# Kernel tuning notes

Measured on AMD Instinct MI355X. Metric: run time of the kernel, lower is better.

Reference implementation:

```python
import jax, jax.numpy as jnp
import numpy as np

IOU_HI = 0.5
IOU_LO = 0.0
ROI_BS = 256
POS_RATIO = 0.25
BG = 20  # background class id; valid classes 0..BG-1
NUM_POS = int(ROI_BS * POS_RATIO)
DELTAS_SCALING = np.array([10.0, 10.0, 5.0, 5.0], dtype=np.float32)  # (x, y, w, h)


def _make_boxes(key, shape):
    ka, kb = jax.random.split(key)
    c = jax.random.uniform(ka, shape + (2,), minval=0.05, maxval=0.95)
    s = jax.random.uniform(kb, shape + (2,), minval=0.02, maxval=0.4)
    lo = jnp.clip(c - s / 2, 0.0, 1.0)
    hi = jnp.clip(c + s / 2, 0.0, 1.0)
    return jnp.concatenate([lo, hi], -1)  # (y1, x1, y2, x2), normalized


def setup_inputs() -> dict:
    key = jax.random.key(0)
    k1, k2, k3 = jax.random.split(key, 3)
    B, N, G = 32, 12000, 200
    rois = _make_boxes(k1, (B, N))
    gt_boxes = _make_boxes(k2, (B, G))
    # class == BG marks a padded / invalid GT box
    gt_class_ids = jax.random.randint(k3, (B, G), 0, BG + 1).astype(jnp.int32)
    return {"rois": rois, "gt_class_ids": gt_class_ids, "gt_boxes": gt_boxes}


def _iou(rois, gts):
    # rois [N,4], gts [G,4] in (y1,x1,y2,x2) -> [N,G]
    y1 = jnp.maximum(rois[:, None, 0], gts[None, :, 0])
    x1 = jnp.maximum(rois[:, None, 1], gts[None, :, 1])
    y2 = jnp.minimum(rois[:, None, 2], gts[None, :, 2])
    x2 = jnp.minimum(rois[:, None, 3], gts[None, :, 3])
    inter = jnp.clip(y2 - y1, 0.0) * jnp.clip(x2 - x1, 0.0)
    ar = (rois[:, 2] - rois[:, 0]) * (rois[:, 3] - rois[:, 1])
    ag = (gts[:, 2] - gts[:, 0]) * (gts[:, 3] - gts[:, 1])
    return inter / (ar[:, None] + ag[None, :] - inter + 1e-8)


def _encode(r, g):
    # (tx, ty, tw, th) * scaling, r/g: [K,4] in (y1,x1,y2,x2)
    eps = 1e-6
    rh = r[:, 2] - r[:, 0]; rw = r[:, 3] - r[:, 1]
    rcy = r[:, 0] + rh / 2; rcx = r[:, 1] + rw / 2
    gh = g[:, 2] - g[:, 0]; gw = g[:, 3] - g[:, 1]
    gcy = g[:, 0] + gh / 2; gcx = g[:, 1] + gw / 2
    tx = (gcx - rcx) / (rw + eps)
    ty = (gcy - rcy) / (rh + eps)
    tw = jnp.log(jnp.maximum(gw, eps) / (rw + eps))
    th = jnp.log(jnp.maximum(gh, eps) / (rh + eps))
    return jnp.stack([tx, ty, tw, th], -1) * jnp.asarray(DELTAS_SCALING)


def _per_image(rois, gt_cls, gt_boxes):
    iou = _iou(rois, gt_boxes)                       # [N,G]
    valid_gt = gt_cls < BG
    iou = jnp.where(valid_gt[None, :], iou, -1.0)
    max_iou = iou.max(1)                             # [N]
    best_gt = iou.argmax(1)                          # [N]
    pos = max_iou >= IOU_HI
    neg = (max_iou < IOU_HI) & (max_iou >= IOU_LO)

    # deterministic sampling: highest-IoU positives / negatives first
    pos_val, pos_idx = jax.lax.top_k(jnp.where(pos, max_iou, -1.0), NUM_POS)
    pos_ok = pos_val > 0.0
    neg_val, neg_idx = jax.lax.top_k(jnp.where(neg, max_iou + 2.0, -1.0), ROI_BS)
    neg_ok = neg_val > 0.0

    rP = jnp.arange(NUM_POS, dtype=jnp.float32)
    rN = jnp.arange(ROI_BS, dtype=jnp.float32)
    prio = jnp.concatenate([jnp.where(pos_ok, 1e9 - rP, -1e9 - rP),
                            jnp.where(neg_ok, 1e6 - rN, -1e6 - rN)])
    cand_idx = jnp.concatenate([pos_idx, neg_idx])
    cand_pos = jnp.concatenate([pos_ok, jnp.zeros(ROI_BS, bool)])
    _, sel = jax.lax.top_k(prio, ROI_BS)
    sel_roi = cand_idx[sel]                          # [ROI_BS]
    sel_is_pos = cand_pos[sel]                       # [ROI_BS]

    labels = jnp.where(sel_is_pos, gt_cls[best_gt[sel_roi]], BG)
    rois_sel = rois[sel_roi]                         # [ROI_BS,4]
    gts_sel = gt_boxes[best_gt[sel_roi]]             # [ROI_BS,4]
    t = _encode(rois_sel, gts_sel) * sel_is_pos[:, None].astype(rois.dtype)

    cls_onehot = jax.nn.one_hot(labels, BG + 1, dtype=rois.dtype)   # [ROI_BS,BG+1]
    onehot_fg = jax.nn.one_hot(labels, BG, dtype=rois.dtype)        # zero row for bg
    mask4 = jnp.repeat(onehot_fg, 4, axis=1)                        # [ROI_BS,4*BG]
    deltas_full = (onehot_fg[:, :, None] * t[:, None, :]).reshape(ROI_BS, 4 * BG)
    reg = jnp.concatenate([mask4, deltas_full], -1)                 # [ROI_BS,8*BG]
    return rois_sel, cls_onehot, reg


def reference(rois, gt_class_ids, gt_boxes):
    return jax.vmap(_per_image)(rois, gt_class_ids, gt_boxes)
```

## Files before the change

### kernel.cpp

```cpp
#include <hip/hip_runtime.h>
#include <stdint.h>

#pragma clang fp contract(off)

#define BATCH 32
#define NROI  12000
#define NGT   200
#define BGCLS 20
#define ROIBS 256
#define NPOS  64
#define NBIN  1024
#define CAP   1024
#define NPAD  256
#define TSEL  1024
#define HSH   16
#define HST   (NBIN + 2)

__device__ __forceinline__ void roi_maxiou_all(const float4* cbox, const float* carea,
                                               int nv, float ry1, float rx1,
                                               float ry2, float rx2,
                                               float& best, int& bj) {
#pragma clang fp contract(off)
  float ar = (ry2 - ry1) * (rx2 - rx1);
  best = -1.0f; bj = 0;
  for (int j = 0; j < nv; ++j) {
    float4 q = cbox[j];
    float yy1 = fmaxf(ry1, q.x);
    float xx1 = fmaxf(rx1, q.y);
    float yy2 = fminf(ry2, q.z);
    float xx2 = fminf(rx2, q.w);
    float inter = fmaxf(yy2 - yy1, 0.0f) * fmaxf(xx2 - xx1, 0.0f);
    float den = ((ar + carea[j]) - inter) + 1e-8f;
    float iou = inter / den;
    if (iou > best) { best = iou; bj = j; }
  }
}

__global__ __launch_bounds__(256) void k_ioumax(const float* __restrict__ rois,
                                                const int* __restrict__ gtc,
                                                const float* __restrict__ gtb,
                                                float* __restrict__ max_iou,
                                                int* __restrict__ best_j) {
#pragma clang fp contract(off)
  __shared__ float4 cbox[NPAD];
  __shared__ float carea[NPAD];
  __shared__ int snv, wtmp[4];
  const int b = blockIdx.y;
  const int tid = threadIdx.x;

  cbox[tid] = make_float4(2.f, 2.f, 2.f, 2.f);
  carea[tid] = 0.f;
  {
    bool valid = false; float4 p = make_float4(0.f, 0.f, 0.f, 0.f);
    if (tid < NGT) {
      p = *(const float4*)(gtb + ((size_t)b * NGT + tid) * 4);
      valid = gtc[(size_t)b * NGT + tid] < BGCLS;
    }
    unsigned long long m = __ballot(valid);
    int w = tid >> 6;
    if ((tid & 63) == 0) wtmp[w] = __popcll(m);
    __syncthreads();
    if (tid == 0) snv = wtmp[0] + wtmp[1] + wtmp[2] + wtmp[3];
    if (valid) {
      int off = 0;
      for (int i = 0; i < w; ++i) off += wtmp[i];
      int pos = off + __popcll(m & ((1ull << (tid & 63)) - 1ull));
      cbox[pos] = p;
      carea[pos] = (p.z - p.x) * (p.w - p.y);
    }
    __syncthreads();
  }
  const int nv = snv;

  int n = blockIdx.x * 256 + tid;
  if (n >= NROI) return;
  const float4 r = *(const float4*)(rois + ((size_t)b * NROI + n) * 4);
  const float ar = (r.z - r.x) * (r.w - r.y);
  float best = -1.0f; int bj = 0;
#pragma unroll 1
  for (int c = 0; c < 4; ++c) {
    unsigned long long m = 0ull;
#pragma unroll 8
    for (int j2 = 0; j2 < 64; ++j2) {
      float4 q = cbox[c * 64 + j2];
      bool ov = (fminf(r.z, q.z) > fmaxf(r.x, q.x)) &&
                (fminf(r.w, q.w) > fmaxf(r.y, q.y));
      m |= ((unsigned long long)ov) << j2;
    }
    while (m) {
      int j2 = __ffsll(m) - 1;
      m &= (m - 1);
      int j = c * 64 + j2;
      float4 q = cbox[j];
      float yy1 = fmaxf(r.x, q.x);
      float xx1 = fmaxf(r.y, q.y);
      float yy2 = fminf(r.z, q.z);
      float xx2 = fminf(r.w, q.w);
      float inter = fmaxf(yy2 - yy1, 0.0f) * fmaxf(xx2 - xx1, 0.0f);
      float den = ((ar + carea[j]) - inter) + 1e-8f;
      float iou = inter / den;
      if (iou > best) { best = iou; bj = j; }
    }
  }
  if (best < 0.0f && nv > 0) best = 0.0f;
  max_iou[(size_t)b * NROI + n] = best;
  best_j[(size_t)b * NROI + n] = bj;
}

template <bool USE_WS>
__global__ __launch_bounds__(TSEL) void k_sel(const float* __restrict__ rois,
                                              const int* __restrict__ gtc,
                                              const float* __restrict__ gtb,
                                              const float* __restrict__ max_iou,
                                              const int* __restrict__ best_j,
                                              float* __restrict__ out) {
#pragma clang fp contract(off)
  __shared__ float4 cbox[NGT];
  __shared__ float carea[NGT];
  __shared__ int ccls[NGT];
  __shared__ int snv, wtmp[16];
  __shared__ float val[NROI];
  __shared__ unsigned long long list[CAP];
  __shared__ int hs[HSH][HST];
  __shared__ int ss[NBIN];
  __shared__ int sel_r[ROIBS];
  __shared__ int scnt, sT;
  const int b = blockIdx.x;
  const int tid = threadIdx.x;

  {
    bool valid = false; float4 p = make_float4(0.f, 0.f, 0.f, 0.f); int cls = BGCLS;
    if (tid < NGT) {
      p = *(const float4*)(gtb + ((size_t)b * NGT + tid) * 4);
      cls = gtc[(size_t)b * NGT + tid];
      valid = (cls < BGCLS);
    }
    unsigned long long m = __ballot(valid);
    int w = tid >> 6;
    if ((tid & 63) == 0) wtmp[w] = __popcll(m);
    if (tid < ROIBS) sel_r[tid] = 0;
    __syncthreads();
    if (tid == 0) { int s = 0; for (int i = 0; i < 16; ++i) s += wtmp[i]; snv = s; }
    if (valid) {
      int off = 0;
      for (int i = 0; i < w; ++i) off += wtmp[i];
      int pos = off + __popcll(m & ((1ull << (tid & 63)) - 1ull));
      cbox[pos] = p;
      carea[pos] = (p.z - p.x) * (p.w - p.y);
      ccls[pos] = cls;
    }
    __syncthreads();
  }
  const int nv = snv;

  if constexpr (USE_WS) {
    for (int n = tid; n < NROI; n += TSEL) val[n] = max_iou[(size_t)b * NROI + n];
  } else {
    for (int n = tid; n < NROI; n += TSEL) {
      const float4 r = *(const float4*)(rois + ((size_t)b * NROI + n) * 4);
      float best; int bj;
      roi_maxiou_all(cbox, carea, nv, r.x, r.y, r.z, r.w, best, bj);
      val[n] = best;
    }
  }
  __syncthreads();

  auto phase = [&](bool isPos, int need, unsigned base, int shift,
                   float lo, float hi, int slotBase) -> int {
    for (int i = tid; i < HSH * HST; i += TSEL) ((int*)hs)[i] = 0;
    if (tid == 0) { scnt = 0; sT = 0; }
    __syncthreads();
    const int sh = tid & (HSH - 1);
    for (int n = tid; n < NROI; n += TSEL) {
      float v = val[n];
      if (v >= lo && v < hi) {
        float kv = isPos ? v : (v + 2.0f);
        int bin = min((int)((__float_as_uint(kv) - base) >> shift), NBIN - 1);
        atomicAdd(&hs[sh][bin], 1);
      }
    }
    __syncthreads();
    {
      int s = 0;
#pragma unroll
      for (int i = 0; i < HSH; ++i) s += hs[i][tid];
      ss[tid] = s;
    }
    __syncthreads();
    for (int off = 1; off < NBIN; off <<= 1) {
      int a = (tid + off < NBIN) ? ss[tid + off] : 0;
      __syncthreads();
      ss[tid] += a;
      __syncthreads();
    }
    {
      int nxt = (tid + 1 < NBIN) ? ss[tid + 1] : 0;
      if (ss[tid] >= need && nxt < need) sT = tid;
    }
    __syncthreads();
    const int T = sT;
    for (int n = tid; n < NROI; n += TSEL) {
      float v = val[n];
      if (v >= lo && v < hi) {
        unsigned kh = __float_as_uint(isPos ? v : (v + 2.0f));
        int bin = min((int)((kh - base) >> shift), NBIN - 1);
        if (bin >= T) {
          int idx = atomicAdd(&scnt, 1);
          if (idx < CAP)
            list[idx] = ((unsigned long long)kh << 32) | (unsigned)(0x7fffffff - n);
        }
      }
    }
    __syncthreads();
    const int cnt = min(scnt, CAP);
    const int limit = min(cnt, need);
    if (tid < cnt) {
      unsigned long long ki = list[tid];
      int rank = 0;
      for (int j = 0; j < cnt; ++j) rank += (list[j] > ki);
      if (rank < limit)
        sel_r[slotBase + rank] = 0x7fffffff - (int)(ki & 0xffffffffu);
    }
    __syncthreads();
    return limit;
  };

  const int P = phase(true, NPOS, 0x3F000000u, 13, 0.5f, 3.0f, 0);
  phase(false, ROIBS - P, 0x40000000u, 11, 0.0f, 0.5f, P);

  {
    const int slot = tid >> 2, q = tid & 3;
    const int r = sel_r[slot];
    const int isp = (slot < P) ? 1 : 0;
    const float4 rv = *(const float4*)(rois + ((size_t)b * NROI + r) * 4);
    float ry1 = rv.x, rx1 = rv.y, ry2 = rv.z, rx2 = rv.w;
    int bj;
    if constexpr (USE_WS) {
      bj = best_j[(size_t)b * NROI + r];
    } else {
      float bb;
      roi_maxiou_all(cbox, carea, nv, ry1, rx1, ry2, rx2, bb, bj);
    }
    int label = isp ? ccls[bj] : BGCLS;

    float* out1 = out;
    float* out2 = out + (size_t)BATCH * ROIBS * 4;
    float* out3 = out + (size_t)BATCH * ROIBS * 25;
    size_t row = (size_t)b * ROIBS + slot;

    if (q == 0) {
      *(float4*)(out1 + row * 4) = rv;
      float* o2 = out2 + row * 21;
      for (int c = 0; c <= BGCLS; ++c) o2[c] = (c == label) ? 1.0f : 0.0f;
    }

    float t0 = 0.f, t1 = 0.f, t2 = 0.f, t3 = 0.f;
    if (isp) {
      const float eps = 1e-6f;
      float4 g = cbox[bj];
      float gy1 = g.x, gx1 = g.y, gy2 = g.z, gx2 = g.w;
      float rh = ry2 - ry1, rw = rx2 - rx1;
      float rcy = ry1 + rh * 0.5f, rcx = rx1 + rw * 0.5f;
      float gh = gy2 - gy1, gw = gx2 - gx1;
      float gcy = gy1 + gh * 0.5f, gcx = gx1 + gw * 0.5f;
      t0 = ((gcx - rcx) / (rw + eps)) * 10.0f;
      t1 = ((gcy - rcy) / (rh + eps)) * 10.0f;
      t2 = logf(fmaxf(gw, eps) / (rw + eps)) * 5.0f;
      t3 = logf(fmaxf(gh, eps) / (rh + eps)) * 5.0f;
    }
    int m0 = label * 4;
    float* o3 = out3 + row * 160;
    for (int c = q * 10; c < q * 10 + 10; ++c) {
      float4 wv = make_float4(0.f, 0.f, 0.f, 0.f);
      if (isp) {
        float* wp = &wv.x;
#pragma unroll
        for (int jj = 0; jj < 4; ++jj) {
          int e = c * 4 + jj;
          float x = 0.f;
          if (e >= m0 && e < m0 + 4) x = 1.0f;
          int d = e - 80 - m0;
          if (d == 0) x = t0; else if (d == 1) x = t1;
          else if (d == 2) x = t2; else if (d == 3) x = t3;
          wp[jj] = x;
        }
      }
      *(float4*)(o3 + c * 4) = wv;
    }
  }
}

extern "C" void kernel_launch(void* const* d_in, const int* in_sizes, int n_in,
                              void* d_out, int out_size, void* d_ws, size_t ws_size,
                              hipStream_t stream) {
  const float* rois = (const float*)d_in[0];
  const int*   gtc  = (const int*)d_in[1];
  const float* gtb  = (const float*)d_in[2];
  float*       out  = (float*)d_out;

  size_t need = (size_t)BATCH * NROI * 8;
  if (d_ws && ws_size >= need) {
    float* mi = (float*)d_ws;
    int*   bj = (int*)d_ws + (size_t)BATCH * NROI;
    k_ioumax<<<dim3((NROI + 255) / 256, BATCH), 256, 0, stream>>>(rois, gtc, gtb, mi, bj);
    k_sel<true><<<BATCH, TSEL, 0, stream>>>(rois, gtc, gtb, mi, bj, out);
  } else {
    k_sel<false><<<BATCH, TSEL, 0, stream>>>(rois, gtc, gtb, nullptr, nullptr, out);
  }
}
```

Baseline: 100.7 us.

## Use fast-reciprocal dense IoU argmax with exact fallback and wave-level suffix scan

The IoU max kernel swaps the ballot-mask sparse overlap loop for a dense loop over the valid GT boxes. Each IoU is computed with a hardware reciprocal, and the kernel tracks the top two values. When the top two are too close to separate given the reciprocal's error, it recomputes exactly via roi_maxiou_all; otherwise it recomputes only the winner with a true division. The selection kernel replaces the 10-step shared-memory Hillis-Steele suffix scan, which needs two barriers per step, with a wavefront shuffle scan plus a 16-entry cross-wave combine. This cuts barriers and LDS traffic. The dense loop does more arithmetic than the sparse one and adds a divergent fallback path.

```diff
diff --git a/kernel.cpp b/kernel.cpp
--- a/kernel.cpp
+++ b/kernel.cpp
@@ -11,7 +11,6 @@
 #define NPOS  64
 #define NBIN  1024
 #define CAP   1024
-#define NPAD  256
 #define TSEL  1024
 #define HSH   16
 #define HST   (NBIN + 2)
@@ -42,14 +41,12 @@
                                                 float* __restrict__ max_iou,
                                                 int* __restrict__ best_j) {
 #pragma clang fp contract(off)
-  __shared__ float4 cbox[NPAD];
-  __shared__ float carea[NPAD];
+  __shared__ float4 cbox[NGT];
+  __shared__ float carea[NGT];
   __shared__ int snv, wtmp[4];
   const int b = blockIdx.y;
   const int tid = threadIdx.x;
 
-  cbox[tid] = make_float4(2.f, 2.f, 2.f, 2.f);
-  carea[tid] = 0.f;
   {
     bool valid = false; float4 p = make_float4(0.f, 0.f, 0.f, 0.f);
     if (tid < NGT) {
@@ -76,33 +73,42 @@
   if (n >= NROI) return;
   const float4 r = *(const float4*)(rois + ((size_t)b * NROI + n) * 4);
   const float ar = (r.z - r.x) * (r.w - r.y);
-  float best = -1.0f; int bj = 0;
-#pragma unroll 1
-  for (int c = 0; c < 4; ++c) {
-    unsigned long long m = 0ull;
-#pragma unroll 8
-    for (int j2 = 0; j2 < 64; ++j2) {
-      float4 q = cbox[c * 64 + j2];
-      bool ov = (fminf(r.z, q.z) > fmaxf(r.x, q.x)) &&
-                (fminf(r.w, q.w) > fmaxf(r.y, q.y));
-      m |= ((unsigned long long)ov) << j2;
-    }
-    while (m) {
-      int j2 = __ffsll(m) - 1;
-      m &= (m - 1);
-      int j = c * 64 + j2;
+
+  float best; int bj;
+  if (nv == 0) {
+    best = -1.0f; bj = 0;
+  } else {
+    float v1 = -1.0f, v2 = -2.0f; int j1 = 0;
+#pragma unroll 2
+    for (int j = 0; j < nv; ++j) {
       float4 q = cbox[j];
+      float ag = carea[j];
       float yy1 = fmaxf(r.x, q.x);
       float xx1 = fmaxf(r.y, q.y);
       float yy2 = fminf(r.z, q.z);
       float xx2 = fminf(r.w, q.w);
       float inter = fmaxf(yy2 - yy1, 0.0f) * fmaxf(xx2 - xx1, 0.0f);
-      float den = ((ar + carea[j]) - inter) + 1e-8f;
-      float iou = inter / den;
-      if (iou > best) { best = iou; bj = j; }
-    }
-  }
-  if (best < 0.0f && nv > 0) best = 0.0f;
+      float den = ((ar + ag) - inter) + 1e-8f;
+      float a = inter * __builtin_amdgcn_rcpf(den);
+      bool gt = a > v1;
+      v2 = gt ? v1 : fmaxf(v2, a);
+      j1 = gt ? j : j1;
+      v1 = gt ? a : v1;
+    }
+    if (v2 >= v1 * 0.999995f) {
+      roi_maxiou_all(cbox, carea, nv, r.x, r.y, r.z, r.w, best, bj);
+    } else {
+      float4 q = cbox[j1];
+      float yy1 = fmaxf(r.x, q.x);
+      float xx1 = fmaxf(r.y, q.y);
+      float yy2 = fminf(r.z, q.z);
+      float xx2 = fminf(r.w, q.w);
+      float inter = fmaxf(yy2 - yy1, 0.0f) * fmaxf(xx2 - xx1, 0.0f);
+      float den = ((ar + carea[j1]) - inter) + 1e-8f;
+      best = inter / den;
+      bj = j1;
+    }
+  }
   max_iou[(size_t)b * NROI + n] = best;
   best_j[(size_t)b * NROI + n] = bj;
 }
@@ -119,6 +125,7 @@
   __shared__ float carea[NGT];
   __shared__ int ccls[NGT];
   __shared__ int snv, wtmp[16];
+  __shared__ int wtot[16], wnext[16];
   __shared__ float val[NROI];
   __shared__ unsigned long long list[CAP];
   __shared__ int hs[HSH][HST];
@@ -180,22 +187,30 @@
       }
     }
     __syncthreads();
-    {
+    int cnt_bin = 0;
+#pragma unroll
+    for (int i = 0; i < HSH; ++i) cnt_bin += hs[i][tid];
+    const int lane = tid & 63, w = tid >> 6;
+    int sfx = cnt_bin;
+#pragma unroll
+    for (int off = 1; off < 64; off <<= 1) {
+      int t = __shfl_down(sfx, off, 64);
+      sfx += (lane + off < 64) ? t : 0;
+    }
+    if (lane == 0) wtot[w] = sfx;
+    __syncthreads();
+    if (tid < 16) {
       int s = 0;
-#pragma unroll
-      for (int i = 0; i < HSH; ++i) s += hs[i][tid];
-      ss[tid] = s;
-    }
-    __syncthreads();
-    for (int off = 1; off < NBIN; off <<= 1) {
-      int a = (tid + off < NBIN) ? ss[tid + off] : 0;
-      __syncthreads();
-      ss[tid] += a;
-      __syncthreads();
-    }
+      for (int i = tid + 1; i < 16; ++i) s += wtot[i];
+      wnext[tid] = s;
+    }
+    __syncthreads();
+    const int suffix = sfx + wnext[w];
+    ss[tid] = suffix;
+    __syncthreads();
     {
       int nxt = (tid + 1 < NBIN) ? ss[tid + 1] : 0;
-      if (ss[tid] >= need && nxt < need) sT = tid;
+      if (suffix >= need && nxt < need) sT = tid;
     }
     __syncthreads();
     const int T = sT;
```

After: 86.33 us. 1.17x faster.
